# Performance work log

Measured on AMD Instinct MI355X. Metric: run time of the kernel, lower is better.

The kernel has to match this reference:

```python
import jax, jax.numpy as jnp
import numpy as np
from jax import lax

B, T, D = 8, 4096, 1024


def setup_inputs() -> dict:
    key = jax.random.key(0)
    ks = jax.random.split(key, 8)
    s = 1.0 / np.sqrt(D)  # keep GEMM outputs O(1)
    return {
        "x": jax.random.normal(ks[0], (B, T, D), dtype=jnp.float32),
        "state_p": jnp.zeros((B, D), dtype=jnp.float32),
        "decay": 0.8 + 0.19 * jax.random.uniform(ks[1], (D,), dtype=jnp.float32),  # ~0.9, stable
        "mass": jnp.ones((D,), dtype=jnp.float32),
        "Wq": s * jax.random.normal(ks[2], (D, D), dtype=jnp.float32),
        "bq": jnp.zeros((D,), dtype=jnp.float32),
        "Wk": s * jax.random.normal(ks[3], (D, D), dtype=jnp.float32),
        "bk": jnp.zeros((D,), dtype=jnp.float32),
        "Wv": s * jax.random.normal(ks[4], (D, D), dtype=jnp.float32),
        "bv": jnp.zeros((D,), dtype=jnp.float32),
    }


def reference(x, state_p, decay, mass, Wq, bq, Wk, bk, Wv, bv):
    # Batch all per-timestep projections into single GEMMs over (B*T) tokens.
    k_logit = jnp.einsum("btd,ed->bte", x, Wk) + bk        # [B,T,D]
    v = jnp.einsum("btd,ed->bte", x, Wv) + bv              # [B,T,D]
    u = jax.nn.sigmoid(k_logit) * v                          # gated input, [B,T,D]

    # Diagonal linear recurrence p_t = decay * p_{t-1} + u_t via scan over time.
    def step(p, u_t):
        p = p * decay + u_t
        return p, p

    final_p, ps = lax.scan(step, state_p, jnp.swapaxes(u, 0, 1))  # ps: [T,B,D]
    p = jnp.swapaxes(ps, 0, 1)                                     # [B,T,D]

    velocities = (jnp.einsum("btd,ed->bte", p, Wq) + bq) / mass    # [B,T,D]
    return velocities, final_p
```

## Files before the change

kernel.cpp:

```cpp
#include <hip/hip_runtime.h>
#include <stdint.h>
#include <stddef.h>

#define D_DIM 1024
#define T_LEN 4096
#define B_SZ 8
#define M_ROWS 32768
#define KTOT 1024
#define CHUNK 64
#define NCHUNK 64

typedef unsigned short u16;
typedef unsigned short u16x8 __attribute__((ext_vector_type(8)));
typedef __bf16 bf16x8 __attribute__((ext_vector_type(8)));
typedef float f32x4 __attribute__((ext_vector_type(4)));

__device__ __forceinline__ u16 f2bf(float f) {
    union { float f; unsigned u; } v; v.f = f;
    unsigned r = v.u + 0x7fffu + ((v.u >> 16) & 1u);
    return (u16)(r >> 16);
}
__device__ __forceinline__ float bf2f(u16 h) {
    union { unsigned u; float f; } v; v.u = ((unsigned)h) << 16;
    return v.f;
}

__global__ void convert_all_kernel(const float* __restrict__ x,
                                   const float* __restrict__ Wk, const float* __restrict__ Wv,
                                   const float* __restrict__ Wq,
                                   u16* __restrict__ xb, u16* __restrict__ wcat,
                                   u16* __restrict__ wqb) {
    const int NX = (M_ROWS * D_DIM) / 4;
    const int total = NX + 3072 * 256;
    int stride = gridDim.x * blockDim.x;
    for (int j = blockIdx.x * blockDim.x + threadIdx.x; j < total; j += stride) {
        const float4* s4;
        ushort4* d4;
        if (j < NX) {
            s4 = (const float4*)x + j;
            d4 = (ushort4*)xb + j;
        } else {
            int idx = j - NX;
            int r = idx >> 8, c4 = idx & 255;
            if (r < 2048) {
                int g = r >> 5, jj = r & 31;
                s4 = (const float4*)((jj < 16 ? Wk : Wv) + (size_t)(g * 16 + (jj & 15)) * D_DIM) + c4;
                d4 = (ushort4*)(wcat + (size_t)r * D_DIM) + c4;
            } else {
                s4 = (const float4*)(Wq + (size_t)(r - 2048) * D_DIM) + c4;
                d4 = (ushort4*)(wqb + (size_t)(r - 2048) * D_DIM) + c4;
            }
        }
        float4 v = *s4;
        ushort4 o;
        o.x = f2bf(v.x); o.y = f2bf(v.y); o.z = f2bf(v.z); o.w = f2bf(v.w);
        *d4 = o;
    }
}

__device__ __forceinline__ void gload16(const u16* g, u16* l) {
    __builtin_amdgcn_global_load_lds(
        (const __attribute__((address_space(1))) void*)g,
        (__attribute__((address_space(3))) void*)l,
        16, 0, 0);
}

template<bool CAT>
__global__ __launch_bounds__(512, 2) void gemm16_kernel(
    const u16* __restrict__ A,
    const u16* __restrict__ Bg,
    const float* __restrict__ bias0,
    const float* __restrict__ bias1,
    u16* __restrict__ Uout,
    float* __restrict__ Fout,
    const float* __restrict__ decay,
    float* __restrict__ localc)
{
    constexpr int NT = KTOT / 64;
    __shared__ u16 smem[2 * 32768];

    const int tid  = threadIdx.x;
    const int w    = tid >> 6;
    const int lane = tid & 63;

    const int cpx = gridDim.x >> 3;
    const int swz = (blockIdx.x & 7) * cpx + (blockIdx.x >> 3);
    const int nCol = CAT ? 8 : 4;
    const int M0 = (swz / nCol) * 256;
    const int N0 = (swz % nCol) * 256;

    const int srow = lane >> 2;
    const int sg   = (lane & 3) ^ ((srow >> 1) & 3);

    const u16* pA0 = A  + (size_t)(M0 + w * 32 +      srow) * KTOT + sg * 8;
    const u16* pA1 = A  + (size_t)(M0 + w * 32 + 16 + srow) * KTOT + sg * 8;
    const u16* pB0 = Bg + (size_t)(N0 + w * 32 +      srow) * KTOT + sg * 8;
    const u16* pB1 = Bg + (size_t)(N0 + w * 32 + 16 + srow) * KTOT + sg * 8;

    auto stA = [&](u16* nxt, int h) {
        gload16(pA0, nxt + h * 8192 + w * 1024);       pA0 += 32;
        gload16(pA1, nxt + h * 8192 + w * 1024 + 512); pA1 += 32;
    };
    auto stB = [&](u16* nxt, int h) {
        gload16(pB0, nxt + 16384 + h * 8192 + w * 1024);       pB0 += 32;
        gload16(pB1, nxt + 16384 + h * 8192 + w * 1024 + 512); pB1 += 32;
    };

    const int wrow = (w >> 2) * 128;
    const int wcol = (w & 3) * 64;
    const int fr = lane & 15;
    const int fq = lane >> 4;

    int offA[8], offB[4];
#pragma unroll
    for (int m = 0; m < 8; ++m) {
        int row = wrow + m * 16 + fr;
        offA[m] = row * 32 + ((fq ^ ((row >> 1) & 3)) << 3);
    }
#pragma unroll
    for (int n = 0; n < 4; ++n) {
        int row = wcol + n * 16 + fr;
        offB[n] = 16384 + row * 32 + ((fq ^ ((row >> 1) & 3)) << 3);
    }

    f32x4 acc[8][4] = {};
    bf16x8 aA[4], aB[4], aC[4], aD[4], bA[4], bC[4];

    stA(smem, 0); stB(smem, 0); stA(smem, 1); stB(smem, 1);
    asm volatile("s_waitcnt vmcnt(4)" ::: "memory");
    __builtin_amdgcn_s_barrier();
#pragma unroll
    for (int m = 0; m < 4; ++m) aA[m] = *(const bf16x8*)(smem + offA[m]);
#pragma unroll
    for (int n = 0; n < 4; ++n) bA[n] = *(const bf16x8*)(smem + offB[n]);

#pragma unroll 1
    for (int t = 0; t < NT; ++t) {
        const u16* cur = smem + (t & 1) * 32768;
        u16* nxt = smem + ((t + 1) & 1) * 32768;
        const bool pf = (t + 1 < NT);

#pragma unroll
        for (int m = 0; m < 4; ++m) aB[m] = *(const bf16x8*)(cur + offA[4 + m]);
        if (pf) stA(nxt, 0);
#pragma unroll
        for (int m = 0; m < 4; ++m)
#pragma unroll
            for (int n = 0; n < 4; ++n)
                acc[m][n] = __builtin_amdgcn_mfma_f32_16x16x32_bf16(aA[m], bA[n], acc[m][n], 0, 0, 0);

        if (pf) { asm volatile("s_waitcnt vmcnt(2)" ::: "memory"); }
        else    { asm volatile("s_waitcnt vmcnt(0)" ::: "memory"); }
        __builtin_amdgcn_s_barrier();
#pragma unroll
        for (int m = 0; m < 4; ++m) aC[m] = *(const bf16x8*)(cur + 8192 + offA[m]);
#pragma unroll
        for (int n = 0; n < 4; ++n) bC[n] = *(const bf16x8*)(cur + 8192 + offB[n]);
        if (pf) stB(nxt, 0);
#pragma unroll
        for (int m = 0; m < 4; ++m)
#pragma unroll
            for (int n = 0; n < 4; ++n)
                acc[4 + m][n] = __builtin_amdgcn_mfma_f32_16x16x32_bf16(aB[m], bA[n], acc[4 + m][n], 0, 0, 0);

#pragma unroll
        for (int m = 0; m < 4; ++m) aD[m] = *(const bf16x8*)(cur + 8192 + offA[4 + m]);
        if (pf) stA(nxt, 1);
#pragma unroll
        for (int m = 0; m < 4; ++m)
#pragma unroll
            for (int n = 0; n < 4; ++n)
                acc[m][n] = __builtin_amdgcn_mfma_f32_16x16x32_bf16(aC[m], bC[n], acc[m][n], 0, 0, 0);

        if (pf) { asm volatile("s_waitcnt vmcnt(2)" ::: "memory"); }
        __builtin_amdgcn_s_barrier();
        if (pf) {
#pragma unroll
            for (int m = 0; m < 4; ++m) aA[m] = *(const bf16x8*)(nxt + offA[m]);
#pragma unroll
            for (int n = 0; n < 4; ++n) bA[n] = *(const bf16x8*)(nxt + offB[n]);
            stB(nxt, 1);
        }
#pragma unroll
        for (int m = 0; m < 4; ++m)
#pragma unroll
            for (int n = 0; n < 4; ++n)
                acc[4 + m][n] = __builtin_amdgcn_mfma_f32_16x16x32_bf16(aD[m], bC[n], acc[4 + m][n], 0, 0, 0);
    }

    if (CAT) {
        asm volatile("s_waitcnt lgkmcnt(0) vmcnt(0)" ::: "memory");
        __syncthreads();
        u16 (*uld)[128] = (u16(*)[128])smem;
        const int ucol0 = N0 / 2;
#pragma unroll
        for (int m = 0; m < 8; ++m) {
#pragma unroll
            for (int p = 0; p < 2; ++p) {
                int lcol = (w & 3) * 32 + p * 16 + fr;
                float b0 = bias0[ucol0 + lcol];
                float b1 = bias1[ucol0 + lcol];
#pragma unroll
                for (int j = 0; j < 4; ++j) {
                    int row = wrow + m * 16 + fq * 4 + j;
                    float kl = acc[m][2 * p][j] + b0;
                    float vv = acc[m][2 * p + 1][j] + b1;
                    float sig = 1.0f / (1.0f + __expf(-kl));
                    uld[row][lcol ^ (((row >> 2) & 3) << 4)] = f2bf(sig * vv);
                }
            }
        }
        __syncthreads();
#pragma unroll
        for (int g = 0; g < 8; ++g) {
            int idx = tid + g * 512;
            int row = idx >> 4, grp = idx & 15;
            int lcol = (grp * 8) ^ (((row >> 2) & 3) << 4);
            *(u16x8*)(Uout + (size_t)(M0 + row) * D_DIM + ucol0 + grp * 8) =
                *(const u16x8*)&uld[row][lcol];
        }
        {
            int chunk = tid >> 7;
            int col   = tid & 127;
            float dec = decay[ucol0 + col];
            float carry = 0.f;
#pragma unroll 4
            for (int s = 0; s < 64; ++s) {
                int r = chunk * 64 + s;
                carry = fmaf(carry, dec, bf2f(uld[r][col ^ (((r >> 2) & 3) << 4)]));
            }
            localc[(size_t)(M0 / 64 + chunk) * D_DIM + ucol0 + col] = carry;
        }
    } else {
#pragma unroll
        for (int n = 0; n < 4; ++n) {
            int col = N0 + wcol + n * 16 + fr;
            float b0 = bias0[col];
            float b1 = bias1[col];
#pragma unroll
            for (int m = 0; m < 8; ++m) {
                int row0 = M0 + wrow + m * 16 + fq * 4;
#pragma unroll
                for (int j = 0; j < 4; ++j)
                    Fout[(size_t)(row0 + j) * D_DIM + col] = (acc[m][n][j] + b0) / b1;
            }
        }
    }
}

__global__ void carry_scan_kernel(const float* __restrict__ localc, const float* __restrict__ state_p,
                                  const float* __restrict__ decay, float* __restrict__ prefix,
                                  float* __restrict__ final_p) {
    int id = blockIdx.x * blockDim.x + threadIdx.x;
    int d = id & (D_DIM - 1);
    int b = id >> 10;
    float dec = decay[d];
    float dl = dec;
#pragma unroll
    for (int i = 0; i < 6; ++i) dl *= dl;
    float P = state_p[id];
    for (int c = 0; c < NCHUNK; ++c) {
        int idx = (b * NCHUNK + c) * D_DIM + d;
        prefix[idx] = P;
        P = fmaf(P, dl, localc[idx]);
    }
    final_p[id] = P;
}

__global__ void reconstruct_kernel(u16* __restrict__ u, const float* __restrict__ decay,
                                   const float* __restrict__ prefix) {
    int id = blockIdx.x * blockDim.x + threadIdx.x;
    int d8 = id & 127;
    int c  = (id >> 7) & (NCHUNK - 1);
    int b  = id >> 13;
    float4 dlo = ((const float4*)decay)[d8 * 2];
    float4 dhi = ((const float4*)decay)[d8 * 2 + 1];
    float dec[8] = {dlo.x, dlo.y, dlo.z, dlo.w, dhi.x, dhi.y, dhi.z, dhi.w};
    const float* pf = prefix + ((size_t)(b * NCHUNK + c)) * D_DIM + d8 * 8;
    float p[8];
#pragma unroll
    for (int j = 0; j < 8; ++j) p[j] = pf[j];
    u16* up = u + ((size_t)b * T_LEN + (size_t)c * CHUNK) * D_DIM + d8 * 8;
    for (int s = 0; s < CHUNK; ++s) {
        u16x8 v = *(const u16x8*)(up + (size_t)s * D_DIM);
        u16x8 o;
#pragma unroll
        for (int j = 0; j < 8; ++j) {
            p[j] = fmaf(p[j], dec[j], bf2f(v[j]));
            o[j] = f2bf(p[j]);
        }
        *(u16x8*)(up + (size_t)s * D_DIM) = o;
    }
}

extern "C" void kernel_launch(void* const* d_in, const int* in_sizes, int n_in,
                              void* d_out, int out_size, void* d_ws, size_t ws_size,
                              hipStream_t stream) {
    const float* x       = (const float*)d_in[0];
    const float* state_p = (const float*)d_in[1];
    const float* decay   = (const float*)d_in[2];
    const float* mass    = (const float*)d_in[3];
    const float* Wq      = (const float*)d_in[4];
    const float* bq      = (const float*)d_in[5];
    const float* Wk      = (const float*)d_in[6];
    const float* bk      = (const float*)d_in[7];
    const float* Wv      = (const float*)d_in[8];
    const float* bv      = (const float*)d_in[9];

    float* out     = (float*)d_out;
    float* final_p = out + (size_t)M_ROWS * D_DIM;

    u16* xb = (u16*)d_out;

    u16* wcat = (u16*)d_ws;
    u16* wqb  = wcat + 2048 * 1024;
    u16* ub   = wqb + 1024 * 1024;
    float* localc = (float*)(ub + (size_t)M_ROWS * D_DIM);
    float* prefix = localc + B_SZ * NCHUNK * D_DIM;

    convert_all_kernel<<<4096, 256, 0, stream>>>(x, Wk, Wv, Wq, xb, wcat, wqb);

    gemm16_kernel<true><<<dim3(1024), dim3(512), 0, stream>>>(
        xb, wcat, bk, bv, ub, nullptr, decay, localc);

    carry_scan_kernel<<<32, 256, 0, stream>>>(localc, state_p, decay, prefix, final_p);
    reconstruct_kernel<<<256, 256, 0, stream>>>(ub, decay, prefix);

    gemm16_kernel<false><<<dim3(512), dim3(512), 0, stream>>>(
        ub, wqb, bq, mass, nullptr, out, nullptr, nullptr);
}
```

Before: 293.4 us.

## Parallelize chunk-carry scan across chunks and raise wave priority around MFMA blocks

The carry scan kernel previously ran 32 blocks where each thread walked 64 chunks serially. It now launches 512 blocks of 1024 threads and does a Hillis-Steele parallel scan over chunks in shared memory, composing (gain, value) pairs. This removes a long serial latency chain from a very low-occupancy kernel, at the cost of more barriers and shared-memory traffic. Separately, the GEMM kernel wraps each MFMA block in s_setprio(1)/s_setprio(0) so waves issuing matrix ops get scheduling priority over waves issuing loads.

```diff
diff --git a/kernel.cpp b/kernel.cpp
--- a/kernel.cpp
+++ b/kernel.cpp
@@ -66,7 +66,7 @@
 }
 
 template<bool CAT>
-__global__ __launch_bounds__(512, 2) void gemm16_kernel(
+__global__ __launch_bounds__(512, 2) void gemm17_kernel(
     const u16* __restrict__ A,
     const u16* __restrict__ Bg,
     const float* __restrict__ bias0,
@@ -143,11 +143,13 @@
 #pragma unroll
         for (int m = 0; m < 4; ++m) aB[m] = *(const bf16x8*)(cur + offA[4 + m]);
         if (pf) stA(nxt, 0);
+        __builtin_amdgcn_s_setprio(1);
 #pragma unroll
         for (int m = 0; m < 4; ++m)
 #pragma unroll
             for (int n = 0; n < 4; ++n)
                 acc[m][n] = __builtin_amdgcn_mfma_f32_16x16x32_bf16(aA[m], bA[n], acc[m][n], 0, 0, 0);
+        __builtin_amdgcn_s_setprio(0);
 
         if (pf) { asm volatile("s_waitcnt vmcnt(2)" ::: "memory"); }
         else    { asm volatile("s_waitcnt vmcnt(0)" ::: "memory"); }
@@ -157,20 +159,24 @@
 #pragma unroll
         for (int n = 0; n < 4; ++n) bC[n] = *(const bf16x8*)(cur + 8192 + offB[n]);
         if (pf) stB(nxt, 0);
+        __builtin_amdgcn_s_setprio(1);
 #pragma unroll
         for (int m = 0; m < 4; ++m)
 #pragma unroll
             for (int n = 0; n < 4; ++n)
                 acc[4 + m][n] = __builtin_amdgcn_mfma_f32_16x16x32_bf16(aB[m], bA[n], acc[4 + m][n], 0, 0, 0);
+        __builtin_amdgcn_s_setprio(0);
 
 #pragma unroll
         for (int m = 0; m < 4; ++m) aD[m] = *(const bf16x8*)(cur + 8192 + offA[4 + m]);
         if (pf) stA(nxt, 1);
+        __builtin_amdgcn_s_setprio(1);
 #pragma unroll
         for (int m = 0; m < 4; ++m)
 #pragma unroll
             for (int n = 0; n < 4; ++n)
                 acc[m][n] = __builtin_amdgcn_mfma_f32_16x16x32_bf16(aC[m], bC[n], acc[m][n], 0, 0, 0);
+        __builtin_amdgcn_s_setprio(0);
 
         if (pf) { asm volatile("s_waitcnt vmcnt(2)" ::: "memory"); }
         __builtin_amdgcn_s_barrier();
@@ -181,11 +187,13 @@
             for (int n = 0; n < 4; ++n) bA[n] = *(const bf16x8*)(nxt + offB[n]);
             stB(nxt, 1);
         }
+        __builtin_amdgcn_s_setprio(1);
 #pragma unroll
         for (int m = 0; m < 4; ++m)
 #pragma unroll
             for (int n = 0; n < 4; ++n)
                 acc[4 + m][n] = __builtin_amdgcn_mfma_f32_16x16x32_bf16(aD[m], bC[n], acc[4 + m][n], 0, 0, 0);
+        __builtin_amdgcn_s_setprio(0);
     }
 
     if (CAT) {
@@ -248,23 +256,43 @@
     }
 }
 
-__global__ void carry_scan_kernel(const float* __restrict__ localc, const float* __restrict__ state_p,
-                                  const float* __restrict__ decay, float* __restrict__ prefix,
-                                  float* __restrict__ final_p) {
-    int id = blockIdx.x * blockDim.x + threadIdx.x;
-    int d = id & (D_DIM - 1);
-    int b = id >> 10;
+__global__ __launch_bounds__(1024) void carry_scan_kernel(
+    const float* __restrict__ localc, const float* __restrict__ state_p,
+    const float* __restrict__ decay, float* __restrict__ prefix,
+    float* __restrict__ final_p)
+{
+    __shared__ float Vs[64][17], Gs[64][17];
+    const int tid = threadIdx.x;
+    const int c  = tid >> 4;
+    const int dl = tid & 15;
+    const int b  = blockIdx.x >> 6;
+    const int dg = blockIdx.x & 63;
+    const int d  = dg * 16 + dl;
+
     float dec = decay[d];
-    float dl = dec;
-#pragma unroll
-    for (int i = 0; i < 6; ++i) dl *= dl;
-    float P = state_p[id];
-    for (int c = 0; c < NCHUNK; ++c) {
-        int idx = (b * NCHUNK + c) * D_DIM + d;
-        prefix[idx] = P;
-        P = fmaf(P, dl, localc[idx]);
-    }
-    final_p[id] = P;
+    float g = dec;
+#pragma unroll
+    for (int i = 0; i < 6; ++i) g *= g;
+    float v = localc[(size_t)(b * NCHUNK + c) * D_DIM + d];
+    Vs[c][dl] = v; Gs[c][dl] = g;
+    __syncthreads();
+#pragma unroll
+    for (int s = 1; s < 64; s <<= 1) {
+        float lv = 0.f, lg = 1.f;
+        if (c >= s) { lv = Vs[c - s][dl]; lg = Gs[c - s][dl]; }
+        __syncthreads();
+        if (c >= s) {
+            float sv = Vs[c][dl], sgg = Gs[c][dl];
+            Vs[c][dl] = fmaf(lv, sgg, sv);
+            Gs[c][dl] = lg * sgg;
+        }
+        __syncthreads();
+    }
+    float P0 = state_p[b * D_DIM + d];
+    float pref = (c == 0) ? P0 : fmaf(P0, Gs[c - 1][dl], Vs[c - 1][dl]);
+    prefix[(size_t)(b * NCHUNK + c) * D_DIM + d] = pref;
+    if (c == 63)
+        final_p[b * D_DIM + d] = fmaf(P0, Gs[63][dl], Vs[63][dl]);
 }
 
 __global__ void reconstruct_kernel(u16* __restrict__ u, const float* __restrict__ decay,
@@ -320,12 +348,12 @@
 
     convert_all_kernel<<<4096, 256, 0, stream>>>(x, Wk, Wv, Wq, xb, wcat, wqb);
 
-    gemm16_kernel<true><<<dim3(1024), dim3(512), 0, stream>>>(
+    gemm17_kernel<true><<<dim3(1024), dim3(512), 0, stream>>>(
         xb, wcat, bk, bv, ub, nullptr, decay, localc);
 
-    carry_scan_kernel<<<32, 256, 0, stream>>>(localc, state_p, decay, prefix, final_p);
+    carry_scan_kernel<<<512, 1024, 0, stream>>>(localc, state_p, decay, prefix, final_p);
     reconstruct_kernel<<<256, 256, 0, stream>>>(ub, decay, prefix);
 
-    gemm16_kernel<false><<<dim3(512), dim3(512), 0, stream>>>(
+    gemm17_kernel<false><<<dim3(512), dim3(512), 0, stream>>>(
         ub, wqb, bq, mass, nullptr, out, nullptr, nullptr);
 }
```

New measurement: 294.4 us. No clear change (+0.3%).
